# Kernel tuning notes

Hardware: AMD Instinct MI355X
Metric: run time of the kernel (lower is better)

Reference implementation:

```python
import jax, jax.numpy as jnp
import numpy as np

DIM = 768
HEADS = 12
HEAD_DIM = DIM // HEADS  # 64, must equal 2*ROPE_DIM
HIDDEN = int(DIM * 4 * 2 / 3)  # 2048
EPS = 1e-6


def _ln(x, w, b, eps=EPS):
    mu = jnp.mean(x, -1, keepdims=True)
    var = jnp.mean((x - mu) ** 2, -1, keepdims=True)
    return (x - mu) * jax.lax.rsqrt(var + eps) * w + b


def _rotate_half(x):
    xr = x.reshape(x.shape[:-1] + (-1, 2))
    return jnp.stack((-xr[..., 1], xr[..., 0]), -1).reshape(x.shape)


def _rope_tables(H, W):
    # Matches get_rope: dim=32 per axis, pt_seq_len=16, theta=10000
    dim, pt, theta = 32, 16.0, 10000.0
    freqs = 1.0 / theta ** (np.arange(0, dim, 2, dtype=np.float32) / dim)  # [16]
    fH = np.repeat((np.arange(H, dtype=np.float32) / H * pt)[:, None] * freqs[None, :], 2, axis=-1)  # [H,32]
    fW = np.repeat((np.arange(W, dtype=np.float32) / W * pt)[:, None] * freqs[None, :], 2, axis=-1)  # [W,32]
    f = np.concatenate([np.broadcast_to(fH[:, None, :], (H, W, dim)),
                        np.broadcast_to(fW[None, :, :], (H, W, dim))], -1)  # [H,W,64]
    f = f.reshape(H * W, 2 * dim)
    return jnp.asarray(np.cos(f)), jnp.asarray(np.sin(f))


def block_forward(x, ln1_w, ln1_b, q_w, q_b, k_w, v_w, v_b, proj_w, proj_b,
                  ln2_w, ln2_b, w1_w, w1_b, w2_w, w2_b, ffn_w, ffn_b, w3_w, w3_b, ws):
    B, H, W, C = x.shape
    shortcut = x
    h = _ln(x, ln1_w, ln1_b)
    # window partition with padding
    pad_h = (-H) % ws
    pad_w = (-W) % ws
    h = jnp.pad(h, ((0, 0), (0, pad_h), (0, pad_w), (0, 0)))
    Hp, Wp = H + pad_h, W + pad_w
    h = h.reshape(B, Hp // ws, ws, Wp // ws, ws, C).transpose(0, 1, 3, 2, 4, 5).reshape(-1, ws, ws, C)
    Bw = h.shape[0]
    N = ws * ws
    t = h.reshape(Bw, N, C)
    q = t @ q_w + q_b  # k has no bias
    k = t @ k_w
    v = t @ v_w + v_b
    q = q.reshape(Bw, N, HEADS, HEAD_DIM).transpose(0, 2, 1, 3)  # [Bw,h,N,d]
    k = k.reshape(Bw, N, HEADS, HEAD_DIM).transpose(0, 2, 1, 3)
    v = v.reshape(Bw, N, HEADS, HEAD_DIM).transpose(0, 2, 1, 3)
    cos, sin = _rope_tables(ws, ws)  # [N, 64]
    q = q * cos + _rotate_half(q) * sin
    k = k * cos + _rotate_half(k) * sin
    scale = HEAD_DIM ** (-0.5)
    attn = jax.nn.softmax(jnp.einsum('bhnd,bhmd->bhnm', q * scale, k), axis=-1)
    o = jnp.einsum('bhnm,bhmd->bhnd', attn, v).transpose(0, 2, 1, 3).reshape(Bw, N, -1)
    o = o @ proj_w + proj_b
    o = o.reshape(Bw, ws, ws, C)
    # window unpartition
    o = o.reshape(B, Hp // ws, Wp // ws, ws, ws, C).transpose(0, 1, 3, 2, 4, 5).reshape(B, Hp, Wp, C)
    o = o[:, :H, :W, :]
    x = shortcut + o
    # SwiGLU MLP with sub-LN
    h = _ln(x, ln2_w, ln2_b)
    hid = jax.nn.silu(h @ w1_w + w1_b) * (h @ w2_w + w2_b)
    hid = _ln(hid, ffn_w, ffn_b)
    return x + hid @ w3_w + w3_b


def setup_inputs() -> dict:
    key = jax.random.key(0)
    ks = jax.random.split(key, 9)
    s = 0.02
    d = {
        'x': jax.random.normal(ks[0], (8, 64, 64, DIM), jnp.float32),
        'ln1_w': jnp.ones((DIM,), jnp.float32),
        'ln1_b': jnp.zeros((DIM,), jnp.float32),
        'q_w': jax.random.normal(ks[1], (DIM, DIM), jnp.float32) * s,
        'q_b': jnp.zeros((DIM,), jnp.float32),
        'k_w': jax.random.normal(ks[2], (DIM, DIM), jnp.float32) * s,
        'v_w': jax.random.normal(ks[3], (DIM, DIM), jnp.float32) * s,
        'v_b': jnp.zeros((DIM,), jnp.float32),
        'proj_w': jax.random.normal(ks[4], (DIM, DIM), jnp.float32) * s,
        'proj_b': jnp.zeros((DIM,), jnp.float32),
        'ln2_w': jnp.ones((DIM,), jnp.float32),
        'ln2_b': jnp.zeros((DIM,), jnp.float32),
        'w1_w': jax.random.normal(ks[5], (DIM, HIDDEN), jnp.float32) * s,
        'w1_b': jnp.zeros((HIDDEN,), jnp.float32),
        'w2_w': jax.random.normal(ks[6], (DIM, HIDDEN), jnp.float32) * s,
        'w2_b': jnp.zeros((HIDDEN,), jnp.float32),
        'ffn_w': jnp.ones((HIDDEN,), jnp.float32),
        'ffn_b': jnp.zeros((HIDDEN,), jnp.float32),
        'w3_w': jax.random.normal(ks[7], (HIDDEN, DIM), jnp.float32) * s,
        'w3_b': jnp.zeros((DIM,), jnp.float32),
        'window_size': 14,
    }
    return d


def reference(x, ln1_w, ln1_b, q_w, q_b, k_w, v_w, v_b, proj_w, proj_b,
              ln2_w, ln2_b, w1_w, w1_b, w2_w, w2_b, ffn_w, ffn_b, w3_w, w3_b, window_size):
    return block_forward(x, ln1_w, ln1_b, q_w, q_b, k_w, v_w, v_b, proj_w, proj_b,
                         ln2_w, ln2_b, w1_w, w1_b, w2_w, w2_b, ffn_w, ffn_b, w3_w, w3_b,
                         int(window_size))
```

## Files before the change

kernel.cpp:

```cpp
#include <hip/hip_runtime.h>
#include <hip/hip_bf16.h>
#include <stdint.h>

typedef unsigned short u16;
typedef unsigned int u32;
typedef __attribute__((ext_vector_type(4))) float f32x4;
typedef __attribute__((ext_vector_type(8))) short s16x8;
typedef __attribute__((ext_vector_type(4))) u32 u32x4;

#define DEV __device__ __forceinline__
#define AS1 __attribute__((address_space(1)))
#define AS3 __attribute__((address_space(3)))

constexpr int T2 = 8 * 64 * 64;
constexpr int C = 768;
constexpr int HID = 2048;
constexpr int CHUNK = 16384;
constexpr int QKVS = 2304;

DEV float blo(u32 u) { return __uint_as_float(u << 16); }
DEV float bhi(u32 u) { return __uint_as_float(u & 0xffff0000u); }
DEV u16 f2bf(float f) {
  u32 x = __float_as_uint(f);
  u32 r = x + 0x7fffu + ((x >> 16) & 1u);
  return (u16)(r >> 16);
}
DEV u32 pack2(float a, float b) { return (u32)f2bf(a) | ((u32)f2bf(b) << 16); }
DEV u32 cvtpk(float lo, float hi) {
  u32 r;
  asm("v_cvt_pk_bf16_f32 %0, %1, %2" : "=v"(r) : "v"(lo), "v"(hi));
  return r;
}

DEV void reduce2(float& s, float& q) {
#pragma unroll
  for (int o = 32; o > 0; o >>= 1) {
    s += __shfl_down(s, o);
    q += __shfl_down(q, o);
  }
  __shared__ float ps[8];
  int wave = threadIdx.x >> 6, lane = threadIdx.x & 63;
  if (lane == 0) { ps[wave] = s; ps[4 + wave] = q; }
  __syncthreads();
  s = ps[0] + ps[1] + ps[2] + ps[3];
  q = ps[4] + ps[5] + ps[6] + ps[7];
}

__global__ __launch_bounds__(256) void transpose_cvt_tiled_k(
    const float* __restrict__ src, u16* __restrict__ dst, int K, int N, int rs, int ro) {
  __shared__ float t[32][33];
  int k0 = blockIdx.x * 32, n0 = blockIdx.y * 32;
  int tx = threadIdx.x, ty = threadIdx.y;
#pragma unroll
  for (int j = 0; j < 4; ++j)
    t[ty + j * 8][tx] = src[(size_t)(k0 + ty + j * 8) * N + n0 + tx];
  __syncthreads();
#pragma unroll
  for (int j = 0; j < 4; ++j) {
    int n = n0 + ty + j * 8;
    dst[((size_t)n * rs + ro) * K + k0 + tx] = f2bf(t[tx][ty + j * 8]);
  }
}

__global__ void build_biases_k(const float* __restrict__ qb, const float* __restrict__ vbb,
                               const float* __restrict__ w1b, const float* __restrict__ w2b,
                               float* __restrict__ qkvb, float* __restrict__ w12b) {
  int i = blockIdx.x * 256 + threadIdx.x;
  if (i < 2304)
    qkvb[i] = i < 768 ? qb[i] : (i < 1536 ? 0.f : vbb[i - 1536]);
  int j = i - 2304;
  if (j >= 0 && j < 4096) w12b[j] = (j & 1) ? w2b[j >> 1] : w1b[j >> 1];
}

__global__ void rope_tables_k(float* __restrict__ ct, float* __restrict__ st) {
  int i = blockIdx.x * 256 + threadIdx.x;
  if (i >= 196 * 32) return;
  int n = i >> 5, jp = i & 31;
  int d = jp << 1;
  int r = n / 14, c = n - r * 14;
  float pos, fj;
  if (d < 32) { pos = (float)r * (16.f / 14.f); fj = (float)(d >> 1); }
  else        { pos = (float)c * (16.f / 14.f); fj = (float)((d - 32) >> 1); }
  float fr = __expf(fj * (-2.f / 32.f) * logf(10000.f));
  float ang = pos * fr;
  float cv = cosf(ang), sv = sinf(ang);
  ct[n * 64 + d] = cv; ct[n * 64 + d + 1] = cv;
  st[n * 64 + d] = sv; st[n * 64 + d + 1] = sv;
}

__global__ __launch_bounds__(256) void ln_k(const float* __restrict__ in,
    const float* __restrict__ w, const float* __restrict__ bb, u16* __restrict__ out) {
  size_t row = blockIdx.x;
  int tid = threadIdx.x;
  const float* xr = in + row * C;
  float v0 = xr[tid], v1 = xr[tid + 256], v2 = xr[tid + 512];
  float s = v0 + v1 + v2, q = v0 * v0 + v1 * v1 + v2 * v2;
  reduce2(s, q);
  float mu = s * (1.f / 768.f), var = q * (1.f / 768.f) - mu * mu;
  float rs = rsqrtf(var + 1e-6f);
  u16* orow = out + row * C;
  orow[tid]       = f2bf((v0 - mu) * rs * w[tid]       + bb[tid]);
  orow[tid + 256] = f2bf((v1 - mu) * rs * w[tid + 256] + bb[tid + 256]);
  orow[tid + 512] = f2bf((v2 - mu) * rs * w[tid + 512] + bb[tid + 512]);
}

DEV float rope1(float v, float p, int r, int d, bool odd, bool isq,
                const float* __restrict__ ct, const float* __restrict__ st) {
  int rem = r & 4095;
  int n = ((rem >> 6) % 14) * 14 + ((rem & 63) % 14);
  float c = ct[n * 64 + d], s = st[n * 64 + d];
  float o = odd ? (v * c + p * s) : (v * c - p * s);
  return isq ? o * 0.125f : o;
}

template <int EPI>
__global__ __launch_bounds__(256) void gemm_k(
    const u16* __restrict__ A, const u16* __restrict__ Bt,
    const float* __restrict__ bias, void* __restrict__ Cout,
    const float* __restrict__ resid, int M, int Nn, int K, int lda,
    const float* __restrict__ ct, const float* __restrict__ st) {
  __shared__ u16 As[128 * 64];
  __shared__ u16 Bs[128 * 64];
  const int tid = threadIdx.x;
  const int wave = tid >> 6, lane = tid & 63;
  const int wm = wave >> 1, wn = wave & 1;
  int tm = blockIdx.x;
  const int gx = gridDim.x;
  if ((gx & 7) == 0) tm = (tm & 7) * (gx >> 3) + (tm >> 3);
  const int tn = blockIdx.y;
  const int l16 = lane & 15, lq = lane >> 4;

  f32x4 acc[4][4];
#pragma unroll
  for (int a = 0; a < 4; ++a)
#pragma unroll
    for (int b = 0; b < 4; ++b)
#pragma unroll
      for (int e = 0; e < 4; ++e) acc[a][b][e] = 0.f;

  const int nk = K >> 6;
  for (int kt = 0; kt < nk; ++kt) {
    const int k0 = kt << 6;
#pragma unroll
    for (int i = 0; i < 4; ++i) {
      int row = (((wave << 2) + i) << 3) + (lane >> 3);
      int cl = (lane & 7) ^ (row & 7);
      const u16* sa = A + (size_t)(tm * 128 + row) * lda + k0 + cl * 8;
      __builtin_amdgcn_global_load_lds((const AS1 u32*)sa,
          (AS3 u32*)(As + (((wave << 2) + i) << 9)), 16, 0, 0);
      const u16* sb = Bt + (size_t)(tn * 128 + row) * K + k0 + cl * 8;
      __builtin_amdgcn_global_load_lds((const AS1 u32*)sb,
          (AS3 u32*)(Bs + (((wave << 2) + i) << 9)), 16, 0, 0);
    }
    asm volatile("s_waitcnt vmcnt(0)" ::: "memory");
    __syncthreads();
#pragma unroll
    for (int ks = 0; ks < 2; ++ks) {
      s16x8 af[4], bfr[4];
#pragma unroll
      for (int mf = 0; mf < 4; ++mf) {
        int row = (wm << 6) + (mf << 4) + l16;
        int sc = ((ks << 2) + lq) ^ (row & 7);
        af[mf] = *(const s16x8*)(As + row * 64 + sc * 8);
      }
#pragma unroll
      for (int nf = 0; nf < 4; ++nf) {
        int row = (wn << 6) + (nf << 4) + l16;
        int sc = ((ks << 2) + lq) ^ (row & 7);
        bfr[nf] = *(const s16x8*)(Bs + row * 64 + sc * 8);
      }
#pragma unroll
      for (int mf = 0; mf < 4; ++mf)
#pragma unroll
        for (int nf = 0; nf < 4; ++nf)
          acc[mf][nf] =
              __builtin_amdgcn_mfma_f32_16x16x32_bf16(af[mf], bfr[nf], acc[mf][nf], 0, 0, 0);
    }
    __syncthreads();
  }

#pragma unroll
  for (int nf = 0; nf < 4; ++nf) {
    int col = (tn << 7) + (wn << 6) + (nf << 4) + l16;
    float bs = bias ? bias[col] : 0.f;
#pragma unroll
    for (int mf = 0; mf < 4; ++mf) {
      int rbase = (tm << 7) + (wm << 6) + (mf << 4) + (lq << 2);
      if constexpr (EPI == 0 || EPI == 3) {
        float v[4];
#pragma unroll
        for (int j = 0; j < 4; ++j) v[j] = acc[mf][nf][j] + bs;
        if constexpr (EPI == 3) {
          float pv[4];
#pragma unroll
          for (int j = 0; j < 4; ++j) pv[j] = __shfl_xor(v[j], 1);
          if (col < 1536) {
            bool odd = (l16 & 1) != 0, isq = col < 768;
            int d = col & 63;
#pragma unroll
            for (int j = 0; j < 4; ++j)
              v[j] = rope1(v[j], pv[j], rbase + j, d, odd, isq, ct, st);
          }
        }
        u32 p01 = cvtpk(v[0], v[1]);
        u32 p23 = cvtpk(v[2], v[3]);
        u16* cp = (u16*)Cout + (size_t)rbase * Nn + col;
        cp[0] = (u16)p01;
        cp[Nn] = (u16)(p01 >> 16);
        cp[2 * Nn] = (u16)p23;
        cp[3 * Nn] = (u16)(p23 >> 16);
      } else {
#pragma unroll
        for (int j = 0; j < 4; ++j) {
          size_t idx = (size_t)(rbase + j) * Nn + col;
          ((float*)Cout)[idx] = resid[idx] + acc[mf][nf][j] + bs;
        }
      }
    }
  }
}

__global__ __launch_bounds__(256) void attn_mfma_k(u16* __restrict__ qkv,
    const float* __restrict__ vb) {
  __shared__ u16 Ks[208 * 64];
  __shared__ u16 Vt[64 * 224];
  __shared__ u16 Pl[4 * 16 * 40];
  u16* q = qkv;
  const u16* k = qkv + 768;
  const u16* v = qkv + 1536;
  int wid = blockIdx.x / 12, h = blockIdx.x - wid * 12;
  int bi = wid / 25, wr = wid - bi * 25;
  int hi = wr / 5, wj = wr - hi * 5;
  int rh = (hi == 4) ? 8 : 14, rw = (wj == 4) ? 8 : 14;
  int nv = rh * rw;
  int nk16 = (nv + 15) >> 4;
  int kvfull = nk16 >> 1;
  int nsteps = kvfull + (nk16 & 1);
  int vcols = ((nk16 + 1) >> 1) << 5;
  int tid = threadIdx.x;
  int rowbase = (bi * 64 + hi * 14) * 64 + wj * 14;

  for (int idx = tid; idx < nk16 * 128; idx += 256) {
    int key = idx >> 3, c = idx & 7;
    u32x4 val = {0, 0, 0, 0};
    if (key < nv) {
      int nr = key / rw, nc = key - nr * rw;
      size_t off = (size_t)(rowbase + nr * 64 + nc) * QKVS + (h << 6) + c * 8;
      val = *(const u32x4*)(k + off);
    }
    int byte = (key * 128 + c * 16) ^ ((key & 7) << 4);
    *(u32x4*)(Ks + (byte >> 1)) = val;
  }
  for (int idx = tid; idx < vcols * 32; idx += 256) {
    int key = idx >> 5, dp = idx & 31;
    int d = dp << 1;
    u32 val;
    if (key < nv) {
      int nr = key / rw, nc = key - nr * rw;
      size_t off = (size_t)(rowbase + nr * 64 + nc) * QKVS + (h << 6) + d;
      val = *(const u32*)(v + off);
    } else {
      val = pack2(vb[(h << 6) + d], vb[(h << 6) + d + 1]);
    }
    int b0 = (d * 448 + key * 2) ^ ((d & 7) << 4);
    int b1 = ((d + 1) * 448 + key * 2) ^ (((d + 1) & 7) << 4);
    Vt[b0 >> 1] = (u16)(val & 0xffffu);
    Vt[b1 >> 1] = (u16)(val >> 16);
  }
  __syncthreads();

  int wave = tid >> 6, lane = tid & 63;
  int l16 = lane & 15, lq = lane >> 4;
  u16* Pw = Pl + wave * 640;
  float vbr[4];
#pragma unroll
  for (int dt = 0; dt < 4; ++dt) vbr[dt] = vb[(h << 6) + dt * 16 + l16];

  int mtiles = (nv + 15) >> 4;
  for (int mt = wave; mt < mtiles; mt += 4) {
    s16x8 a[2];
    {
      int qi = mt * 16 + l16;
      if (qi >= nv) qi = nv - 1;
      int nr = qi / rw, nc = qi - nr * rw;
      const u16* qp = q + (size_t)(rowbase + nr * 64 + nc) * QKVS + (h << 6);
      a[0] = *(const s16x8*)(qp + lq * 8);
      a[1] = *(const s16x8*)(qp + 32 + lq * 8);
    }
    f32x4 O[4];
#pragma unroll
    for (int dt = 0; dt < 4; ++dt)
#pragma unroll
      for (int j = 0; j < 4; ++j) O[dt][j] = 0.f;
    float lrow[4] = {0.f, 0.f, 0.f, 0.f};

    for (int kv = 0; kv < nsteps; ++kv) {
      const bool full = kv < kvfull;
      const int keyb = kv << 5;
      f32x4 s0 = {0.f, 0.f, 0.f, 0.f}, s1 = {0.f, 0.f, 0.f, 0.f};
      int key0 = keyb + l16, key1 = key0 + 16;
#pragma unroll
      for (int s = 0; s < 2; ++s) {
        int byte0 = (key0 * 128 + s * 64 + lq * 16) ^ ((key0 & 7) << 4);
        s16x8 b0 = *(const s16x8*)(Ks + (byte0 >> 1));
        s0 = __builtin_amdgcn_mfma_f32_16x16x32_bf16(a[s], b0, s0, 0, 0, 0);
        if (full) {
          int byte1 = (key1 * 128 + s * 64 + lq * 16) ^ ((key1 & 7) << 4);
          s16x8 b1 = *(const s16x8*)(Ks + (byte1 >> 1));
          s1 = __builtin_amdgcn_mfma_f32_16x16x32_bf16(a[s], b1, s1, 0, 0, 0);
        }
      }
#pragma unroll
      for (int j = 0; j < 4; ++j) {
        float p0 = (key0 < 196) ? __expf(s0[j]) : 0.f;
        float p1 = (full && key1 < 196) ? __expf(s1[j]) : 0.f;
        float rs = p0 + p1;
        rs += __shfl_xor(rs, 1);
        rs += __shfl_xor(rs, 2);
        rs += __shfl_xor(rs, 4);
        rs += __shfl_xor(rs, 8);
        lrow[j] += rs;
        u32 pk = cvtpk(p0, p1);
        Pw[(lq * 4 + j) * 40 + l16] = (u16)pk;
        Pw[(lq * 4 + j) * 40 + l16 + 16] = (u16)(pk >> 16);
      }
      s16x8 pa = *(const s16x8*)(Pw + l16 * 40 + lq * 8);
#pragma unroll
      for (int dt = 0; dt < 4; ++dt) {
        int d = dt * 16 + l16;
        int vbyte = (d * 448 + keyb * 2 + lq * 16) ^ ((d & 7) << 4);
        s16x8 bv = *(const s16x8*)(Vt + (vbyte >> 1));
        O[dt] = __builtin_amdgcn_mfma_f32_16x16x32_bf16(pa, bv, O[dt], 0, 0, 0);
      }
    }
    int Prem = 196 - (nk16 << 4);
    if (Prem > 0) {
#pragma unroll
      for (int j = 0; j < 4; ++j) {
        lrow[j] += (float)Prem;
#pragma unroll
        for (int dt = 0; dt < 4; ++dt) O[dt][j] += (float)Prem * vbr[dt];
      }
    }
#pragma unroll
    for (int j = 0; j < 4; ++j) {
      int qi = mt * 16 + lq * 4 + j;
      if (qi < nv) {
        float inv = 1.f / lrow[j];
        int nr = qi / rw, nc = qi - nr * rw;
        u16* op = q + (size_t)(rowbase + nr * 64 + nc) * QKVS + (h << 6);
#pragma unroll
        for (int dt = 0; dt < 4; ++dt) op[dt * 16 + l16] = f2bf(O[dt][j] * inv);
      }
    }
  }
}

__global__ __launch_bounds__(256) void swiglu_ln_k(u16* __restrict__ h12,
    const float* __restrict__ w, const float* __restrict__ bb) {
  size_t row = blockIdx.x;
  int tid = threadIdx.x;
  const u32x4 ua = *(const u32x4*)(h12 + row * 4096 + tid * 16);
  const u32x4 ub = *(const u32x4*)(h12 + row * 4096 + tid * 16 + 8);
  u32 pp[8] = {ua.x, ua.y, ua.z, ua.w, ub.x, ub.y, ub.z, ub.w};
  float g[8];
  float s = 0.f, qq = 0.f;
#pragma unroll
  for (int j = 0; j < 8; ++j) {
    float a = blo(pp[j]), b = bhi(pp[j]);
    float sl = a / (1.f + __expf(-a));
    g[j] = sl * b;
    s += g[j];
    qq += g[j] * g[j];
  }
  reduce2(s, qq);
  float mu = s * (1.f / 2048.f);
  float var = qq * (1.f / 2048.f) - mu * mu;
  float rs = rsqrtf(var + 1e-6f);
  const float* wp = w + tid * 8;
  const float* bp = bb + tid * 8;
  u32 o4[4];
#pragma unroll
  for (int j = 0; j < 4; ++j) {
    float o0 = (g[2 * j] - mu) * rs * wp[2 * j] + bp[2 * j];
    float o1 = (g[2 * j + 1] - mu) * rs * wp[2 * j + 1] + bp[2 * j + 1];
    o4[j] = cvtpk(o0, o1);
  }
  *(u32x4*)(h12 + row * 4096 + tid * 8) = (u32x4){o4[0], o4[1], o4[2], o4[3]};
}

extern "C" void kernel_launch(void* const* d_in, const int* in_sizes, int n_in,
                              void* d_out, int out_size, void* d_ws, size_t ws_size,
                              hipStream_t stream) {
  const float* x    = (const float*)d_in[0];
  const float* ln1w = (const float*)d_in[1];
  const float* ln1b = (const float*)d_in[2];
  const float* qw   = (const float*)d_in[3];
  const float* qb   = (const float*)d_in[4];
  const float* kw   = (const float*)d_in[5];
  const float* vw   = (const float*)d_in[6];
  const float* vb   = (const float*)d_in[7];
  const float* pw   = (const float*)d_in[8];
  const float* pb   = (const float*)d_in[9];
  const float* ln2w = (const float*)d_in[10];
  const float* ln2b = (const float*)d_in[11];
  const float* w1   = (const float*)d_in[12];
  const float* w1b  = (const float*)d_in[13];
  const float* w2   = (const float*)d_in[14];
  const float* w2b  = (const float*)d_in[15];
  const float* ffw  = (const float*)d_in[16];
  const float* ffb  = (const float*)d_in[17];
  const float* w3   = (const float*)d_in[18];
  const float* w3b  = (const float*)d_in[19];

  char* ws = (char*)d_ws;
  size_t off = 0;
  auto alloc = [&](size_t bytes) -> char* {
    char* p = ws + off;
    off += (bytes + 255) & ~(size_t)255;
    return p;
  };
  u16* qkvwt = (u16*)alloc((size_t)QKVS * 768 * 2);
  u16* pwt   = (u16*)alloc((size_t)768 * 768 * 2);
  u16* w12t  = (u16*)alloc((size_t)4096 * 768 * 2);
  u16* w3t   = (u16*)alloc((size_t)768 * 2048 * 2);
  float* qkvb = (float*)alloc((size_t)QKVS * 4);
  float* w12b = (float*)alloc((size_t)4096 * 4);
  float* ct = (float*)alloc((size_t)196 * 64 * 4);
  float* st = (float*)alloc((size_t)196 * 64 * 4);
  u16* xw  = (u16*)alloc((size_t)T2 * C * 2);
  u16* qkv = (u16*)alloc((size_t)T2 * QKVS * 2);
  u16* h12c = qkv;
  float* x2 = (float*)d_out;

  dim3 tb(32, 8);
  transpose_cvt_tiled_k<<<dim3(24, 24), tb, 0, stream>>>(qw, qkvwt, 768, 768, 1, 0);
  transpose_cvt_tiled_k<<<dim3(24, 24), tb, 0, stream>>>(kw, qkvwt + (size_t)768 * 768, 768, 768, 1, 0);
  transpose_cvt_tiled_k<<<dim3(24, 24), tb, 0, stream>>>(vw, qkvwt + (size_t)1536 * 768, 768, 768, 1, 0);
  transpose_cvt_tiled_k<<<dim3(24, 24), tb, 0, stream>>>(pw, pwt, 768, 768, 1, 0);
  transpose_cvt_tiled_k<<<dim3(24, 64), tb, 0, stream>>>(w1, w12t, 768, 2048, 2, 0);
  transpose_cvt_tiled_k<<<dim3(24, 64), tb, 0, stream>>>(w2, w12t, 768, 2048, 2, 1);
  transpose_cvt_tiled_k<<<dim3(64, 24), tb, 0, stream>>>(w3, w3t, 2048, 768, 1, 0);
  build_biases_k<<<25, 256, 0, stream>>>(qb, vb, w1b, w2b, qkvb, w12b);
  rope_tables_k<<<(196 * 32 + 255) / 256, 256, 0, stream>>>(ct, st);

  ln_k<<<T2, 256, 0, stream>>>(x, ln1w, ln1b, xw);
  gemm_k<3><<<dim3(T2 / 128, QKVS / 128), 256, 0, stream>>>(
      xw, qkvwt, qkvb, qkv, nullptr, T2, QKVS, 768, 768, ct, st);
  attn_mfma_k<<<200 * 12, 256, 0, stream>>>(qkv, vb);
  gemm_k<2><<<dim3(T2 / 128, 6), 256, 0, stream>>>(
      qkv, pwt, pb, x2, x, T2, 768, 768, QKVS, nullptr, nullptr);

  ln_k<<<T2, 256, 0, stream>>>(x2, ln2w, ln2b, xw);
  for (int cidx = 0; cidx < T2 / CHUNK; ++cidx) {
    const u16* hrow = xw + (size_t)cidx * CHUNK * C;
    gemm_k<0><<<dim3(CHUNK / 128, 32), 256, 0, stream>>>(
        hrow, w12t, w12b, h12c, nullptr, CHUNK, 4096, 768, 768, nullptr, nullptr);
    swiglu_ln_k<<<CHUNK, 256, 0, stream>>>(h12c, ffw, ffb);
    gemm_k<2><<<dim3(CHUNK / 128, 6), 256, 0, stream>>>(
        h12c, w3t, w3b, x2 + (size_t)cidx * CHUNK * C,
        x2 + (size_t)cidx * CHUNK * C, CHUNK, 768, 2048, 4096, nullptr, nullptr);
  }
}
```

Baseline: 1.135 ms.

## Remap GEMM tiles per XCD, raise MFMA priority, stream K from global in attention

The GEMM tile mapping now assigns blocks to XCDs in 16-row-tile groups so neighbouring tiles sharing A/B panels land on the same XCD's L2. MFMA sections in the GEMM and attention kernels are wrapped in s_setprio to favour matrix issue. The attention kernel drops the shared-memory K staging and reads K rows straight from global via a precomputed row-index table, which also replaces repeated div/mod address maths. Padded keys beyond nv are now treated as exp(0)=1 inside the loop rather than via zero rows, at the cost of more global loads per key tile.

Result: faster. 1.075 ms (-5.3%).

```diff
diff --git a/kernel.cpp b/kernel.cpp
--- a/kernel.cpp
+++ b/kernel.cpp
@@ -124,10 +124,15 @@
   const int tid = threadIdx.x;
   const int wave = tid >> 6, lane = tid & 63;
   const int wm = wave >> 1, wn = wave & 1;
-  int tm = blockIdx.x;
   const int gx = gridDim.x;
-  if ((gx & 7) == 0) tm = (tm & 7) * (gx >> 3) + (tm >> 3);
-  const int tn = blockIdx.y;
+  const int id = blockIdx.y * gx + blockIdx.x;
+  const int xcd = id & 7;
+  const int j0 = id >> 3;
+  const int per_sub = gridDim.y << 4;
+  const int sub = j0 / per_sub;
+  const int jj = j0 - sub * per_sub;
+  const int tm = xcd * (gx >> 3) + (sub << 4) + (jj & 15);
+  const int tn = jj >> 4;
   const int l16 = lane & 15, lq = lane >> 4;
 
   f32x4 acc[4][4];
@@ -169,12 +174,14 @@
         int sc = ((ks << 2) + lq) ^ (row & 7);
         bfr[nf] = *(const s16x8*)(Bs + row * 64 + sc * 8);
       }
+      __builtin_amdgcn_s_setprio(1);
 #pragma unroll
       for (int mf = 0; mf < 4; ++mf)
 #pragma unroll
         for (int nf = 0; nf < 4; ++nf)
           acc[mf][nf] =
               __builtin_amdgcn_mfma_f32_16x16x32_bf16(af[mf], bfr[nf], acc[mf][nf], 0, 0, 0);
+      __builtin_amdgcn_s_setprio(0);
     }
     __syncthreads();
   }
@@ -222,12 +229,9 @@
 
 __global__ __launch_bounds__(256) void attn_mfma_k(u16* __restrict__ qkv,
     const float* __restrict__ vb) {
-  __shared__ u16 Ks[208 * 64];
   __shared__ u16 Vt[64 * 224];
   __shared__ u16 Pl[4 * 16 * 40];
-  u16* q = qkv;
-  const u16* k = qkv + 768;
-  const u16* v = qkv + 1536;
+  __shared__ int rowTab[208];
   int wid = blockIdx.x / 12, h = blockIdx.x - wid * 12;
   int bi = wid / 25, wr = wid - bi * 25;
   int hi = wr / 5, wj = wr - hi * 5;
@@ -240,25 +244,19 @@
   int tid = threadIdx.x;
   int rowbase = (bi * 64 + hi * 14) * 64 + wj * 14;
 
-  for (int idx = tid; idx < nk16 * 128; idx += 256) {
-    int key = idx >> 3, c = idx & 7;
-    u32x4 val = {0, 0, 0, 0};
-    if (key < nv) {
-      int nr = key / rw, nc = key - nr * rw;
-      size_t off = (size_t)(rowbase + nr * 64 + nc) * QKVS + (h << 6) + c * 8;
-      val = *(const u32x4*)(k + off);
-    }
-    int byte = (key * 128 + c * 16) ^ ((key & 7) << 4);
-    *(u32x4*)(Ks + (byte >> 1)) = val;
-  }
+  if (tid < 208) {
+    int mk = tid < nv ? tid : nv - 1;
+    int nr = mk / rw, nc = mk - nr * rw;
+    rowTab[tid] = rowbase + nr * 64 + nc;
+  }
+  __syncthreads();
   for (int idx = tid; idx < vcols * 32; idx += 256) {
     int key = idx >> 5, dp = idx & 31;
     int d = dp << 1;
     u32 val;
     if (key < nv) {
-      int nr = key / rw, nc = key - nr * rw;
-      size_t off = (size_t)(rowbase + nr * 64 + nc) * QKVS + (h << 6) + d;
-      val = *(const u32*)(v + off);
+      size_t off = (size_t)rowTab[key] * QKVS + 1536 + (h << 6) + d;
+      val = *(const u32*)(qkv + off);
     } else {
       val = pack2(vb[(h << 6) + d], vb[(h << 6) + d + 1]);
     }
@@ -272,6 +270,7 @@
   int wave = tid >> 6, lane = tid & 63;
   int l16 = lane & 15, lq = lane >> 4;
   u16* Pw = Pl + wave * 640;
+  const u16* kbase = qkv + 768 + (h << 6);
   float vbr[4];
 #pragma unroll
   for (int dt = 0; dt < 4; ++dt) vbr[dt] = vb[(h << 6) + dt * 16 + l16];
@@ -281,9 +280,7 @@
     s16x8 a[2];
     {
       int qi = mt * 16 + l16;
-      if (qi >= nv) qi = nv - 1;
-      int nr = qi / rw, nc = qi - nr * rw;
-      const u16* qp = q + (size_t)(rowbase + nr * 64 + nc) * QKVS + (h << 6);
+      const u16* qp = qkv + (size_t)rowTab[qi] * QKVS + (h << 6);
       a[0] = *(const s16x8*)(qp + lq * 8);
       a[1] = *(const s16x8*)(qp + 32 + lq * 8);
     }
@@ -299,21 +296,23 @@
       const int keyb = kv << 5;
       f32x4 s0 = {0.f, 0.f, 0.f, 0.f}, s1 = {0.f, 0.f, 0.f, 0.f};
       int key0 = keyb + l16, key1 = key0 + 16;
+      const u16* kr0 = kbase + (size_t)rowTab[key0] * QKVS;
+      const u16* kr1 = full ? (kbase + (size_t)rowTab[key1] * QKVS) : kbase;
+      __builtin_amdgcn_s_setprio(1);
 #pragma unroll
       for (int s = 0; s < 2; ++s) {
-        int byte0 = (key0 * 128 + s * 64 + lq * 16) ^ ((key0 & 7) << 4);
-        s16x8 b0 = *(const s16x8*)(Ks + (byte0 >> 1));
+        s16x8 b0 = *(const s16x8*)(kr0 + s * 32 + lq * 8);
         s0 = __builtin_amdgcn_mfma_f32_16x16x32_bf16(a[s], b0, s0, 0, 0, 0);
         if (full) {
-          int byte1 = (key1 * 128 + s * 64 + lq * 16) ^ ((key1 & 7) << 4);
-          s16x8 b1 = *(const s16x8*)(Ks + (byte1 >> 1));
+          s16x8 b1 = *(const s16x8*)(kr1 + s * 32 + lq * 8);
           s1 = __builtin_amdgcn_mfma_f32_16x16x32_bf16(a[s], b1, s1, 0, 0, 0);
         }
       }
+      __builtin_amdgcn_s_setprio(0);
 #pragma unroll
       for (int j = 0; j < 4; ++j) {
-        float p0 = (key0 < 196) ? __expf(s0[j]) : 0.f;
-        float p1 = (full && key1 < 196) ? __expf(s1[j]) : 0.f;
+        float p0 = key0 < nv ? __expf(s0[j]) : (key0 < 196 ? 1.f : 0.f);
+        float p1 = full ? (key1 < nv ? __expf(s1[j]) : (key1 < 196 ? 1.f : 0.f)) : 0.f;
         float rs = p0 + p1;
         rs += __shfl_xor(rs, 1);
         rs += __shfl_xor(rs, 2);
@@ -325,6 +324,7 @@
         Pw[(lq * 4 + j) * 40 + l16 + 16] = (u16)(pk >> 16);
       }
       s16x8 pa = *(const s16x8*)(Pw + l16 * 40 + lq * 8);
+      __builtin_amdgcn_s_setprio(1);
 #pragma unroll
       for (int dt = 0; dt < 4; ++dt) {
         int d = dt * 16 + l16;
@@ -332,6 +332,7 @@
         s16x8 bv = *(const s16x8*)(Vt + (vbyte >> 1));
         O[dt] = __builtin_amdgcn_mfma_f32_16x16x32_bf16(pa, bv, O[dt], 0, 0, 0);
       }
+      __builtin_amdgcn_s_setprio(0);
     }
     int Prem = 196 - (nk16 << 4);
     if (Prem > 0) {
@@ -347,8 +348,7 @@
       int qi = mt * 16 + lq * 4 + j;
       if (qi < nv) {
         float inv = 1.f / lrow[j];
-        int nr = qi / rw, nc = qi - nr * rw;
-        u16* op = q + (size_t)(rowbase + nr * 64 + nc) * QKVS + (h << 6);
+        u16* op = qkv + (size_t)rowTab[qi] * QKVS + (h << 6);
 #pragma unroll
         for (int dt = 0; dt < 4; ++dt) op[dt * 16 + l16] = f2bf(O[dt][j] * inv);
       }
```
